# Kernel optimization log

Measured on AMD Instinct MI355X. Metric: run time of the kernel, lower is better.

The kernel has to match this reference:

```python
import jax, jax.numpy as jnp
import numpy as np

N = 50000   # nodes
E = 600000  # edges (avg degree 12)
D = 128     # embedding dim (hardcoded in original: np.zeros(128))
P = 5       # propagation iterations (self.p)


def setup_inputs() -> dict:
    key = jax.random.key(0)
    ks = jax.random.split(key, 10)
    x = jax.random.normal(ks[0], (N, D), jnp.float32)
    g = jax.random.normal(ks[1], (D,), jnp.float32)
    dist = jax.random.uniform(ks[2], (E,), jnp.float32)
    w1 = jax.random.normal(ks[3], (1,), jnp.float32)
    w2 = jax.random.normal(ks[4], (1,), jnp.float32)
    w3 = jax.random.normal(ks[5], (1,), jnp.float32)
    w4 = jax.random.normal(ks[6], (1,), jnp.float32)
    w5 = jax.random.normal(ks[7], (1,), jnp.float32)
    src = jax.random.randint(ks[8], (E,), 0, N)
    dst = jax.random.randint(ks[9], (E,), 0, N)
    return {"x": x, "g": g, "dist": dist, "w1": w1, "w2": w2, "w3": w3,
            "w4": w4, "w5": w5, "src": src, "dst": dst}


def reference(x, g, dist, w1, w2, w3, w4, w5, src, dst):
    # travel_times[i] = sum_{j in N(i)} w5 * dist(i,j)  -- iteration-invariant
    travel = jax.ops.segment_sum(w5[0] * dist, src, num_segments=N)  # [N]
    # per-node affine part, constant across the P iterations
    base = w1[0] * x + w2[0] * g[None, :] + w4[0] * jax.nn.relu(travel)[:, None]  # [N, D]
    u = x  # new_u_vect starts as a copy of x
    for _ in range(P):
        # u_sum[i] = sum_{j in N(i)} u[j]  (gather + segment-sum, synchronous update)
        u_sum = jax.ops.segment_sum(u[dst], src, num_segments=N)  # [N, D]
        u = base + w3[0] * u_sum
    return jax.nn.relu(u)
```

## Files before the change

### kernel.cpp

```cpp
#include <hip/hip_runtime.h>

#define D 128
#define D4 32
#define CAPH 32

typedef float v4f __attribute__((ext_vector_type(4)));
typedef _Float16 h4 __attribute__((ext_vector_type(4)));

static inline size_t align_up(size_t v, size_t a) { return (v + a - 1) & ~(a - 1); }

__global__ void fill_ell_kernel(const int* __restrict__ src,
                                const int* __restrict__ dst,
                                const float* __restrict__ dist,
                                unsigned long long* __restrict__ packedA,
                                unsigned long long* __restrict__ packedB,
                                unsigned short* __restrict__ adjA,
                                unsigned short* __restrict__ adjB,
                                int E, int Ehalf) {
  int e = blockIdx.x * blockDim.x + threadIdx.x;
  if (e >= E) return;
  int s = src[e];
  unsigned long long fx = (unsigned long long)(dist[e] * 4294967296.0f);
  unsigned long long val = (1ull << 48) | fx;
  if (e < Ehalf) {
    unsigned long long old = atomicAdd(&packedA[s], val);
    unsigned int slot = (unsigned int)(old >> 48);
    if (slot < CAPH) adjA[(size_t)s * CAPH + slot] = (unsigned short)dst[e];
  } else {
    unsigned long long old = atomicAdd(&packedB[s], val);
    unsigned int slot = (unsigned int)(old >> 48);
    if (slot < CAPH) adjB[(size_t)s * CAPH + slot] = (unsigned short)dst[e];
  }
}

__global__ void base_seed_kernel(const v4f* __restrict__ x4, const v4f* __restrict__ g4,
                                 const unsigned long long* __restrict__ packedA,
                                 const unsigned long long* __restrict__ packedB,
                                 const float* __restrict__ w1p, const float* __restrict__ w2p,
                                 const float* __restrict__ w4p, const float* __restrict__ w5p,
                                 h4* __restrict__ base, h4* __restrict__ uA,
                                 h4* __restrict__ uB, int n) {
  int i = blockIdx.x * blockDim.x + threadIdx.x;
  int node = i >> 5;
  int lane = i & 31;
  if (node > n) return;
  size_t idx = (size_t)i;
  if (node == n) {
    h4 z = {0, 0, 0, 0};
    uA[idx] = z;
    uB[idx] = z;
    return;
  }
  v4f xv = x4[(size_t)node * D4 + lane];
  v4f gv = g4[lane];
  unsigned long long sum = (packedA[node] & 0xFFFFFFFFFFFFull)
                         + (packedB[node] & 0xFFFFFFFFFFFFull);
  float ds = (float)sum * (1.0f / 4294967296.0f);
  float t = w5p[0] * ds;
  t = t > 0.f ? t : 0.f;
  v4f b = w1p[0] * xv + w2p[0] * gv;
  b += t * w4p[0];
  base[idx] = __builtin_convertvector(b, h4);
  uA[idx] = __builtin_convertvector(xv, h4);
}

__global__ __launch_bounds__(256) void prop_kernel(
    const h4* __restrict__ uin, const h4* __restrict__ base,
    const unsigned long long* __restrict__ packedA,
    const unsigned long long* __restrict__ packedB,
    const unsigned short* __restrict__ adjA,
    const unsigned short* __restrict__ adjB,
    const float* __restrict__ w3p,
    void* __restrict__ uout, int n, int final_relu)
{
  int half  = blockIdx.x & 1;
  int chunk = blockIdx.x >> 1;
  int group = threadIdx.x >> 4;
  int lane  = threadIdx.x & 15;
  int node  = chunk * 16 + group;
  if (node >= n) return;

  unsigned long long pA = packedA[node];
  unsigned long long pB = packedB[node];
  int degA = (int)(pA >> 48); if (degA > CAPH) degA = CAPH;
  int degB = (int)(pB >> 48); if (degB > CAPH) degB = CAPH;

  const unsigned short* rowA = adjA + (size_t)node * CAPH;
  const unsigned short* rowB = adjB + (size_t)node * CAPH;
  int a0 = rowA[lane];
  int a1 = rowA[lane + 16];
  int b0 = rowB[lane];
  int b1 = rowB[lane + 16];

  const h4* uh = uin + (size_t)half * 16 + lane;
  size_t idx = (size_t)node * 32 + half * 16 + lane;
  v4f bb = __builtin_convertvector(base[idx], v4f);

  v4f acc0 = {0.f,0.f,0.f,0.f}, acc1 = acc0, acc2 = acc0, acc3 = acc0;

  {
    int jA0 = __shfl(a0, 0, 16); jA0 = (0 < degA) ? jA0 : n;
    int jA1 = __shfl(a0, 1, 16); jA1 = (1 < degA) ? jA1 : n;
    int jA2 = __shfl(a0, 2, 16); jA2 = (2 < degA) ? jA2 : n;
    int jA3 = __shfl(a0, 3, 16); jA3 = (3 < degA) ? jA3 : n;
    int jA4 = __shfl(a0, 4, 16); jA4 = (4 < degA) ? jA4 : n;
    int jA5 = __shfl(a0, 5, 16); jA5 = (5 < degA) ? jA5 : n;
    int jA6 = __shfl(a0, 6, 16); jA6 = (6 < degA) ? jA6 : n;
    int jA7 = __shfl(a0, 7, 16); jA7 = (7 < degA) ? jA7 : n;
    int jB0 = __shfl(b0, 0, 16); jB0 = (0 < degB) ? jB0 : n;
    int jB1 = __shfl(b0, 1, 16); jB1 = (1 < degB) ? jB1 : n;
    int jB2 = __shfl(b0, 2, 16); jB2 = (2 < degB) ? jB2 : n;
    int jB3 = __shfl(b0, 3, 16); jB3 = (3 < degB) ? jB3 : n;
    int jB4 = __shfl(b0, 4, 16); jB4 = (4 < degB) ? jB4 : n;
    int jB5 = __shfl(b0, 5, 16); jB5 = (5 < degB) ? jB5 : n;
    int jB6 = __shfl(b0, 6, 16); jB6 = (6 < degB) ? jB6 : n;
    int jB7 = __shfl(b0, 7, 16); jB7 = (7 < degB) ? jB7 : n;
    h4 vA0 = uh[(size_t)jA0 * 32];
    h4 vA1 = uh[(size_t)jA1 * 32];
    h4 vA2 = uh[(size_t)jA2 * 32];
    h4 vA3 = uh[(size_t)jA3 * 32];
    h4 vA4 = uh[(size_t)jA4 * 32];
    h4 vA5 = uh[(size_t)jA5 * 32];
    h4 vA6 = uh[(size_t)jA6 * 32];
    h4 vA7 = uh[(size_t)jA7 * 32];
    h4 vB0 = uh[(size_t)jB0 * 32];
    h4 vB1 = uh[(size_t)jB1 * 32];
    h4 vB2 = uh[(size_t)jB2 * 32];
    h4 vB3 = uh[(size_t)jB3 * 32];
    h4 vB4 = uh[(size_t)jB4 * 32];
    h4 vB5 = uh[(size_t)jB5 * 32];
    h4 vB6 = uh[(size_t)jB6 * 32];
    h4 vB7 = uh[(size_t)jB7 * 32];
    acc0 += __builtin_convertvector(vA0, v4f) + __builtin_convertvector(vA1, v4f);
    acc1 += __builtin_convertvector(vA2, v4f) + __builtin_convertvector(vA3, v4f);
    acc2 += __builtin_convertvector(vA4, v4f) + __builtin_convertvector(vA5, v4f);
    acc3 += __builtin_convertvector(vA6, v4f) + __builtin_convertvector(vA7, v4f);
    acc0 += __builtin_convertvector(vB0, v4f) + __builtin_convertvector(vB1, v4f);
    acc1 += __builtin_convertvector(vB2, v4f) + __builtin_convertvector(vB3, v4f);
    acc2 += __builtin_convertvector(vB4, v4f) + __builtin_convertvector(vB5, v4f);
    acc3 += __builtin_convertvector(vB6, v4f) + __builtin_convertvector(vB7, v4f);
  }

  for (int k = 8; k < degA; k += 8) {
    int sel = (k >= 16) ? a1 : a0;
    int j0 = __shfl(sel, (k + 0) & 15, 16); j0 = (k + 0 < degA) ? j0 : n;
    int j1 = __shfl(sel, (k + 1) & 15, 16); j1 = (k + 1 < degA) ? j1 : n;
    int j2 = __shfl(sel, (k + 2) & 15, 16); j2 = (k + 2 < degA) ? j2 : n;
    int j3 = __shfl(sel, (k + 3) & 15, 16); j3 = (k + 3 < degA) ? j3 : n;
    int j4 = __shfl(sel, (k + 4) & 15, 16); j4 = (k + 4 < degA) ? j4 : n;
    int j5 = __shfl(sel, (k + 5) & 15, 16); j5 = (k + 5 < degA) ? j5 : n;
    int j6 = __shfl(sel, (k + 6) & 15, 16); j6 = (k + 6 < degA) ? j6 : n;
    int j7 = __shfl(sel, (k + 7) & 15, 16); j7 = (k + 7 < degA) ? j7 : n;
    h4 v0 = uh[(size_t)j0 * 32];
    h4 v1 = uh[(size_t)j1 * 32];
    h4 v2 = uh[(size_t)j2 * 32];
    h4 v3 = uh[(size_t)j3 * 32];
    h4 v4 = uh[(size_t)j4 * 32];
    h4 v5 = uh[(size_t)j5 * 32];
    h4 v6 = uh[(size_t)j6 * 32];
    h4 v7 = uh[(size_t)j7 * 32];
    acc0 += __builtin_convertvector(v0, v4f) + __builtin_convertvector(v1, v4f);
    acc1 += __builtin_convertvector(v2, v4f) + __builtin_convertvector(v3, v4f);
    acc2 += __builtin_convertvector(v4, v4f) + __builtin_convertvector(v5, v4f);
    acc3 += __builtin_convertvector(v6, v4f) + __builtin_convertvector(v7, v4f);
  }
  for (int k = 8; k < degB; k += 8) {
    int sel = (k >= 16) ? b1 : b0;
    int j0 = __shfl(sel, (k + 0) & 15, 16); j0 = (k + 0 < degB) ? j0 : n;
    int j1 = __shfl(sel, (k + 1) & 15, 16); j1 = (k + 1 < degB) ? j1 : n;
    int j2 = __shfl(sel, (k + 2) & 15, 16); j2 = (k + 2 < degB) ? j2 : n;
    int j3 = __shfl(sel, (k + 3) & 15, 16); j3 = (k + 3 < degB) ? j3 : n;
    int j4 = __shfl(sel, (k + 4) & 15, 16); j4 = (k + 4 < degB) ? j4 : n;
    int j5 = __shfl(sel, (k + 5) & 15, 16); j5 = (k + 5 < degB) ? j5 : n;
    int j6 = __shfl(sel, (k + 6) & 15, 16); j6 = (k + 6 < degB) ? j6 : n;
    int j7 = __shfl(sel, (k + 7) & 15, 16); j7 = (k + 7 < degB) ? j7 : n;
    h4 v0 = uh[(size_t)j0 * 32];
    h4 v1 = uh[(size_t)j1 * 32];
    h4 v2 = uh[(size_t)j2 * 32];
    h4 v3 = uh[(size_t)j3 * 32];
    h4 v4 = uh[(size_t)j4 * 32];
    h4 v5 = uh[(size_t)j5 * 32];
    h4 v6 = uh[(size_t)j6 * 32];
    h4 v7 = uh[(size_t)j7 * 32];
    acc0 += __builtin_convertvector(v0, v4f) + __builtin_convertvector(v1, v4f);
    acc1 += __builtin_convertvector(v2, v4f) + __builtin_convertvector(v3, v4f);
    acc2 += __builtin_convertvector(v4, v4f) + __builtin_convertvector(v5, v4f);
    acc3 += __builtin_convertvector(v6, v4f) + __builtin_convertvector(v7, v4f);
  }
  v4f asum = (acc0 + acc1) + (acc2 + acc3);
  v4f r = bb + w3p[0] * asum;

  if (final_relu) {
    r.x = r.x > 0.f ? r.x : 0.f;
    r.y = r.y > 0.f ? r.y : 0.f;
    r.z = r.z > 0.f ? r.z : 0.f;
    r.w = r.w > 0.f ? r.w : 0.f;
    __builtin_nontemporal_store(r, (v4f*)uout + idx);
  } else {
    ((h4*)uout)[idx] = __builtin_convertvector(r, h4);
  }
}

extern "C" void kernel_launch(void* const* d_in, const int* in_sizes, int n_in,
                              void* d_out, int out_size, void* d_ws, size_t ws_size,
                              hipStream_t stream) {
  const float* x    = (const float*)d_in[0];
  const float* g    = (const float*)d_in[1];
  const float* dist = (const float*)d_in[2];
  const float* w1   = (const float*)d_in[3];
  const float* w2   = (const float*)d_in[4];
  const float* w3   = (const float*)d_in[5];
  const float* w4   = (const float*)d_in[6];
  const float* w5   = (const float*)d_in[7];
  const int*   src  = (const int*)d_in[8];
  const int*   dst  = (const int*)d_in[9];

  const int N = in_sizes[0] / D;
  const int E = in_sizes[2];
  const int Ehalf = E / 2;

  char* ws = (char*)d_ws;
  size_t o = 0;
  unsigned long long* packedA = (unsigned long long*)(ws + o); o += align_up((size_t)N * 8, 256);
  unsigned long long* packedB = (unsigned long long*)(ws + o);
  size_t zero_end = o + (size_t)N * 8;
  o += align_up((size_t)N * 8, 256);
  unsigned short* adjA = (unsigned short*)(ws + o); o += align_up((size_t)N * CAPH * 2, 256);
  unsigned short* adjB = (unsigned short*)(ws + o); o += align_up((size_t)N * CAPH * 2, 256);
  h4* baseB = (h4*)(ws + o); o += align_up((size_t)(N + 1) * D * 2, 256);
  h4* uA    = (h4*)(ws + o); o += align_up((size_t)(N + 1) * D * 2, 256);
  h4* uB    = (h4*)(ws + o); o += align_up((size_t)(N + 1) * D * 2, 256);
  float* out = (float*)d_out;

  hipMemsetAsync(ws, 0, zero_end, stream);

  const int tb = 256;
  const int eblocks = (E + tb - 1) / tb;
  const int sthreads = (N + 1) * 32;
  const int sblocks = (sthreads + tb - 1) / tb;

  fill_ell_kernel<<<eblocks, tb, 0, stream>>>(src, dst, dist, packedA, packedB,
                                              adjA, adjB, E, Ehalf);
  base_seed_kernel<<<sblocks, tb, 0, stream>>>((const v4f*)x, (const v4f*)g,
                                               packedA, packedB,
                                               w1, w2, w4, w5, baseB, uA, uB, N);

  const int chunks = (N + 15) / 16;
  const int pblocks = chunks * 2;
  prop_kernel<<<pblocks, 256, 0, stream>>>(uA, baseB, packedA, packedB, adjA, adjB, w3, uB,  N, 0);
  prop_kernel<<<pblocks, 256, 0, stream>>>(uB, baseB, packedA, packedB, adjA, adjB, w3, uA,  N, 0);
  prop_kernel<<<pblocks, 256, 0, stream>>>(uA, baseB, packedA, packedB, adjA, adjB, w3, uB,  N, 0);
  prop_kernel<<<pblocks, 256, 0, stream>>>(uB, baseB, packedA, packedB, adjA, adjB, w3, uA,  N, 0);
  prop_kernel<<<pblocks, 256, 0, stream>>>(uA, baseB, packedA, packedB, adjA, adjB, w3, out, N, 1);
}
```

Before: 252.6 us.

## Fuse five propagation launches into one persistent kernel with grid barrier

Replaces the five per-iteration prop_kernel launches with one persistent kernel of 768 blocks. Each block owns several node chunks and keeps their adjacency indices, degrees and base values in registers across all iterations. Iterations are separated by an atomic-counter grid barrier held in a zeroed workspace region. This removes launch gaps and repeated loads of per-node metadata, but relies on all 768 blocks being co-resident, which the launch-bounds hint of 3 blocks per CU is meant to ensure. It also raises register pressure and reduces parallelism per iteration.

```diff
diff --git a/kernel.cpp b/kernel.cpp
--- a/kernel.cpp
+++ b/kernel.cpp
@@ -3,6 +3,9 @@
 #define D 128
 #define D4 32
 #define CAPH 32
+#define PITER 5
+#define GBLK 768
+#define CHUNKS 9
 
 typedef float v4f __attribute__((ext_vector_type(4)));
 typedef _Float16 h4 __attribute__((ext_vector_type(4)));
@@ -64,140 +67,180 @@
   uA[idx] = __builtin_convertvector(xv, h4);
 }
 
-__global__ __launch_bounds__(256) void prop_kernel(
-    const h4* __restrict__ uin, const h4* __restrict__ base,
+__global__ __launch_bounds__(256, 3) void prop_persist_kernel(
+    h4* __restrict__ uAb, h4* __restrict__ uBb,
+    const h4* __restrict__ base,
     const unsigned long long* __restrict__ packedA,
     const unsigned long long* __restrict__ packedB,
     const unsigned short* __restrict__ adjA,
     const unsigned short* __restrict__ adjB,
     const float* __restrict__ w3p,
-    void* __restrict__ uout, int n, int final_relu)
+    unsigned* __restrict__ bar,
+    float* __restrict__ out, int n)
 {
   int half  = blockIdx.x & 1;
-  int chunk = blockIdx.x >> 1;
+  int bp    = blockIdx.x >> 1;
   int group = threadIdx.x >> 4;
   int lane  = threadIdx.x & 15;
-  int node  = chunk * 16 + group;
-  if (node >= n) return;
-
-  unsigned long long pA = packedA[node];
-  unsigned long long pB = packedB[node];
-  int degA = (int)(pA >> 48); if (degA > CAPH) degA = CAPH;
-  int degB = (int)(pB >> 48); if (degB > CAPH) degB = CAPH;
-
-  const unsigned short* rowA = adjA + (size_t)node * CAPH;
-  const unsigned short* rowB = adjB + (size_t)node * CAPH;
-  int a0 = rowA[lane];
-  int a1 = rowA[lane + 16];
-  int b0 = rowB[lane];
-  int b1 = rowB[lane + 16];
-
-  const h4* uh = uin + (size_t)half * 16 + lane;
-  size_t idx = (size_t)node * 32 + half * 16 + lane;
-  v4f bb = __builtin_convertvector(base[idx], v4f);
-
-  v4f acc0 = {0.f,0.f,0.f,0.f}, acc1 = acc0, acc2 = acc0, acc3 = acc0;
-
-  {
-    int jA0 = __shfl(a0, 0, 16); jA0 = (0 < degA) ? jA0 : n;
-    int jA1 = __shfl(a0, 1, 16); jA1 = (1 < degA) ? jA1 : n;
-    int jA2 = __shfl(a0, 2, 16); jA2 = (2 < degA) ? jA2 : n;
-    int jA3 = __shfl(a0, 3, 16); jA3 = (3 < degA) ? jA3 : n;
-    int jA4 = __shfl(a0, 4, 16); jA4 = (4 < degA) ? jA4 : n;
-    int jA5 = __shfl(a0, 5, 16); jA5 = (5 < degA) ? jA5 : n;
-    int jA6 = __shfl(a0, 6, 16); jA6 = (6 < degA) ? jA6 : n;
-    int jA7 = __shfl(a0, 7, 16); jA7 = (7 < degA) ? jA7 : n;
-    int jB0 = __shfl(b0, 0, 16); jB0 = (0 < degB) ? jB0 : n;
-    int jB1 = __shfl(b0, 1, 16); jB1 = (1 < degB) ? jB1 : n;
-    int jB2 = __shfl(b0, 2, 16); jB2 = (2 < degB) ? jB2 : n;
-    int jB3 = __shfl(b0, 3, 16); jB3 = (3 < degB) ? jB3 : n;
-    int jB4 = __shfl(b0, 4, 16); jB4 = (4 < degB) ? jB4 : n;
-    int jB5 = __shfl(b0, 5, 16); jB5 = (5 < degB) ? jB5 : n;
-    int jB6 = __shfl(b0, 6, 16); jB6 = (6 < degB) ? jB6 : n;
-    int jB7 = __shfl(b0, 7, 16); jB7 = (7 < degB) ? jB7 : n;
-    h4 vA0 = uh[(size_t)jA0 * 32];
-    h4 vA1 = uh[(size_t)jA1 * 32];
-    h4 vA2 = uh[(size_t)jA2 * 32];
-    h4 vA3 = uh[(size_t)jA3 * 32];
-    h4 vA4 = uh[(size_t)jA4 * 32];
-    h4 vA5 = uh[(size_t)jA5 * 32];
-    h4 vA6 = uh[(size_t)jA6 * 32];
-    h4 vA7 = uh[(size_t)jA7 * 32];
-    h4 vB0 = uh[(size_t)jB0 * 32];
-    h4 vB1 = uh[(size_t)jB1 * 32];
-    h4 vB2 = uh[(size_t)jB2 * 32];
-    h4 vB3 = uh[(size_t)jB3 * 32];
-    h4 vB4 = uh[(size_t)jB4 * 32];
-    h4 vB5 = uh[(size_t)jB5 * 32];
-    h4 vB6 = uh[(size_t)jB6 * 32];
-    h4 vB7 = uh[(size_t)jB7 * 32];
-    acc0 += __builtin_convertvector(vA0, v4f) + __builtin_convertvector(vA1, v4f);
-    acc1 += __builtin_convertvector(vA2, v4f) + __builtin_convertvector(vA3, v4f);
-    acc2 += __builtin_convertvector(vA4, v4f) + __builtin_convertvector(vA5, v4f);
-    acc3 += __builtin_convertvector(vA6, v4f) + __builtin_convertvector(vA7, v4f);
-    acc0 += __builtin_convertvector(vB0, v4f) + __builtin_convertvector(vB1, v4f);
-    acc1 += __builtin_convertvector(vB2, v4f) + __builtin_convertvector(vB3, v4f);
-    acc2 += __builtin_convertvector(vB4, v4f) + __builtin_convertvector(vB5, v4f);
-    acc3 += __builtin_convertvector(vB6, v4f) + __builtin_convertvector(vB7, v4f);
-  }
-
-  for (int k = 8; k < degA; k += 8) {
-    int sel = (k >= 16) ? a1 : a0;
-    int j0 = __shfl(sel, (k + 0) & 15, 16); j0 = (k + 0 < degA) ? j0 : n;
-    int j1 = __shfl(sel, (k + 1) & 15, 16); j1 = (k + 1 < degA) ? j1 : n;
-    int j2 = __shfl(sel, (k + 2) & 15, 16); j2 = (k + 2 < degA) ? j2 : n;
-    int j3 = __shfl(sel, (k + 3) & 15, 16); j3 = (k + 3 < degA) ? j3 : n;
-    int j4 = __shfl(sel, (k + 4) & 15, 16); j4 = (k + 4 < degA) ? j4 : n;
-    int j5 = __shfl(sel, (k + 5) & 15, 16); j5 = (k + 5 < degA) ? j5 : n;
-    int j6 = __shfl(sel, (k + 6) & 15, 16); j6 = (k + 6 < degA) ? j6 : n;
-    int j7 = __shfl(sel, (k + 7) & 15, 16); j7 = (k + 7 < degA) ? j7 : n;
-    h4 v0 = uh[(size_t)j0 * 32];
-    h4 v1 = uh[(size_t)j1 * 32];
-    h4 v2 = uh[(size_t)j2 * 32];
-    h4 v3 = uh[(size_t)j3 * 32];
-    h4 v4 = uh[(size_t)j4 * 32];
-    h4 v5 = uh[(size_t)j5 * 32];
-    h4 v6 = uh[(size_t)j6 * 32];
-    h4 v7 = uh[(size_t)j7 * 32];
-    acc0 += __builtin_convertvector(v0, v4f) + __builtin_convertvector(v1, v4f);
-    acc1 += __builtin_convertvector(v2, v4f) + __builtin_convertvector(v3, v4f);
-    acc2 += __builtin_convertvector(v4, v4f) + __builtin_convertvector(v5, v4f);
-    acc3 += __builtin_convertvector(v6, v4f) + __builtin_convertvector(v7, v4f);
-  }
-  for (int k = 8; k < degB; k += 8) {
-    int sel = (k >= 16) ? b1 : b0;
-    int j0 = __shfl(sel, (k + 0) & 15, 16); j0 = (k + 0 < degB) ? j0 : n;
-    int j1 = __shfl(sel, (k + 1) & 15, 16); j1 = (k + 1 < degB) ? j1 : n;
-    int j2 = __shfl(sel, (k + 2) & 15, 16); j2 = (k + 2 < degB) ? j2 : n;
-    int j3 = __shfl(sel, (k + 3) & 15, 16); j3 = (k + 3 < degB) ? j3 : n;
-    int j4 = __shfl(sel, (k + 4) & 15, 16); j4 = (k + 4 < degB) ? j4 : n;
-    int j5 = __shfl(sel, (k + 5) & 15, 16); j5 = (k + 5 < degB) ? j5 : n;
-    int j6 = __shfl(sel, (k + 6) & 15, 16); j6 = (k + 6 < degB) ? j6 : n;
-    int j7 = __shfl(sel, (k + 7) & 15, 16); j7 = (k + 7 < degB) ? j7 : n;
-    h4 v0 = uh[(size_t)j0 * 32];
-    h4 v1 = uh[(size_t)j1 * 32];
-    h4 v2 = uh[(size_t)j2 * 32];
-    h4 v3 = uh[(size_t)j3 * 32];
-    h4 v4 = uh[(size_t)j4 * 32];
-    h4 v5 = uh[(size_t)j5 * 32];
-    h4 v6 = uh[(size_t)j6 * 32];
-    h4 v7 = uh[(size_t)j7 * 32];
-    acc0 += __builtin_convertvector(v0, v4f) + __builtin_convertvector(v1, v4f);
-    acc1 += __builtin_convertvector(v2, v4f) + __builtin_convertvector(v3, v4f);
-    acc2 += __builtin_convertvector(v4, v4f) + __builtin_convertvector(v5, v4f);
-    acc3 += __builtin_convertvector(v6, v4f) + __builtin_convertvector(v7, v4f);
-  }
-  v4f asum = (acc0 + acc1) + (acc2 + acc3);
-  v4f r = bb + w3p[0] * asum;
-
-  if (final_relu) {
-    r.x = r.x > 0.f ? r.x : 0.f;
-    r.y = r.y > 0.f ? r.y : 0.f;
-    r.z = r.z > 0.f ? r.z : 0.f;
-    r.w = r.w > 0.f ? r.w : 0.f;
-    __builtin_nontemporal_store(r, (v4f*)uout + idx);
-  } else {
-    ((h4*)uout)[idx] = __builtin_convertvector(r, h4);
+  int gg    = bp * 16 + group;
+  const int stride = (GBLK >> 1) * 16;
+
+  float w3 = w3p[0];
+
+  int a0[CHUNKS], a1[CHUNKS], b0[CHUNKS], b1[CHUNKS];
+  int dgA[CHUNKS], dgB[CHUNKS];
+  h4 bs[CHUNKS];
+#pragma unroll
+  for (int c = 0; c < CHUNKS; ++c) {
+    int node = gg + c * stride;
+    bool valid = node < n;
+    int nd = valid ? node : 0;
+    unsigned long long pA = packedA[nd];
+    unsigned long long pB = packedB[nd];
+    int dA = (int)(pA >> 48); if (dA > CAPH) dA = CAPH;
+    int dB = (int)(pB >> 48); if (dB > CAPH) dB = CAPH;
+    dgA[c] = valid ? dA : 0;
+    dgB[c] = valid ? dB : 0;
+    const unsigned short* rowA = adjA + (size_t)nd * CAPH;
+    const unsigned short* rowB = adjB + (size_t)nd * CAPH;
+    a0[c] = rowA[lane];
+    a1[c] = rowA[lane + 16];
+    b0[c] = rowB[lane];
+    b1[c] = rowB[lane + 16];
+    bs[c] = base[(size_t)nd * 32 + half * 16 + lane];
+  }
+
+  for (int it = 0; it < PITER; ++it) {
+    const h4* uin = (it & 1) ? uBb : uAb;
+    h4* uoutp     = (it & 1) ? uAb : uBb;
+    const h4* uh  = uin + (size_t)half * 16 + lane;
+    int last = (it == PITER - 1);
+
+#pragma unroll
+    for (int c = 0; c < CHUNKS; ++c) {
+      int node = gg + c * stride;
+      if (node >= n) break;
+      int degA = dgA[c];
+      int degB = dgB[c];
+
+      v4f acc0 = {0.f,0.f,0.f,0.f}, acc1 = acc0, acc2 = acc0, acc3 = acc0;
+
+      {
+        int jA0 = __shfl(a0[c], 0, 16); jA0 = (0 < degA) ? jA0 : n;
+        int jA1 = __shfl(a0[c], 1, 16); jA1 = (1 < degA) ? jA1 : n;
+        int jA2 = __shfl(a0[c], 2, 16); jA2 = (2 < degA) ? jA2 : n;
+        int jA3 = __shfl(a0[c], 3, 16); jA3 = (3 < degA) ? jA3 : n;
+        int jA4 = __shfl(a0[c], 4, 16); jA4 = (4 < degA) ? jA4 : n;
+        int jA5 = __shfl(a0[c], 5, 16); jA5 = (5 < degA) ? jA5 : n;
+        int jA6 = __shfl(a0[c], 6, 16); jA6 = (6 < degA) ? jA6 : n;
+        int jA7 = __shfl(a0[c], 7, 16); jA7 = (7 < degA) ? jA7 : n;
+        int jB0 = __shfl(b0[c], 0, 16); jB0 = (0 < degB) ? jB0 : n;
+        int jB1 = __shfl(b0[c], 1, 16); jB1 = (1 < degB) ? jB1 : n;
+        int jB2 = __shfl(b0[c], 2, 16); jB2 = (2 < degB) ? jB2 : n;
+        int jB3 = __shfl(b0[c], 3, 16); jB3 = (3 < degB) ? jB3 : n;
+        int jB4 = __shfl(b0[c], 4, 16); jB4 = (4 < degB) ? jB4 : n;
+        int jB5 = __shfl(b0[c], 5, 16); jB5 = (5 < degB) ? jB5 : n;
+        int jB6 = __shfl(b0[c], 6, 16); jB6 = (6 < degB) ? jB6 : n;
+        int jB7 = __shfl(b0[c], 7, 16); jB7 = (7 < degB) ? jB7 : n;
+        h4 vA0 = uh[(size_t)jA0 * 32];
+        h4 vA1 = uh[(size_t)jA1 * 32];
+        h4 vA2 = uh[(size_t)jA2 * 32];
+        h4 vA3 = uh[(size_t)jA3 * 32];
+        h4 vA4 = uh[(size_t)jA4 * 32];
+        h4 vA5 = uh[(size_t)jA5 * 32];
+        h4 vA6 = uh[(size_t)jA6 * 32];
+        h4 vA7 = uh[(size_t)jA7 * 32];
+        h4 vB0 = uh[(size_t)jB0 * 32];
+        h4 vB1 = uh[(size_t)jB1 * 32];
+        h4 vB2 = uh[(size_t)jB2 * 32];
+        h4 vB3 = uh[(size_t)jB3 * 32];
+        h4 vB4 = uh[(size_t)jB4 * 32];
+        h4 vB5 = uh[(size_t)jB5 * 32];
+        h4 vB6 = uh[(size_t)jB6 * 32];
+        h4 vB7 = uh[(size_t)jB7 * 32];
+        acc0 += __builtin_convertvector(vA0, v4f) + __builtin_convertvector(vA1, v4f);
+        acc1 += __builtin_convertvector(vA2, v4f) + __builtin_convertvector(vA3, v4f);
+        acc2 += __builtin_convertvector(vA4, v4f) + __builtin_convertvector(vA5, v4f);
+        acc3 += __builtin_convertvector(vA6, v4f) + __builtin_convertvector(vA7, v4f);
+        acc0 += __builtin_convertvector(vB0, v4f) + __builtin_convertvector(vB1, v4f);
+        acc1 += __builtin_convertvector(vB2, v4f) + __builtin_convertvector(vB3, v4f);
+        acc2 += __builtin_convertvector(vB4, v4f) + __builtin_convertvector(vB5, v4f);
+        acc3 += __builtin_convertvector(vB6, v4f) + __builtin_convertvector(vB7, v4f);
+      }
+
+      for (int k = 8; k < degA; k += 8) {
+        int sel = (k >= 16) ? a1[c] : a0[c];
+        int j0 = __shfl(sel, (k + 0) & 15, 16); j0 = (k + 0 < degA) ? j0 : n;
+        int j1 = __shfl(sel, (k + 1) & 15, 16); j1 = (k + 1 < degA) ? j1 : n;
+        int j2 = __shfl(sel, (k + 2) & 15, 16); j2 = (k + 2 < degA) ? j2 : n;
+        int j3 = __shfl(sel, (k + 3) & 15, 16); j3 = (k + 3 < degA) ? j3 : n;
+        int j4 = __shfl(sel, (k + 4) & 15, 16); j4 = (k + 4 < degA) ? j4 : n;
+        int j5 = __shfl(sel, (k + 5) & 15, 16); j5 = (k + 5 < degA) ? j5 : n;
+        int j6 = __shfl(sel, (k + 6) & 15, 16); j6 = (k + 6 < degA) ? j6 : n;
+        int j7 = __shfl(sel, (k + 7) & 15, 16); j7 = (k + 7 < degA) ? j7 : n;
+        h4 v0 = uh[(size_t)j0 * 32];
+        h4 v1 = uh[(size_t)j1 * 32];
+        h4 v2 = uh[(size_t)j2 * 32];
+        h4 v3 = uh[(size_t)j3 * 32];
+        h4 v4 = uh[(size_t)j4 * 32];
+        h4 v5 = uh[(size_t)j5 * 32];
+        h4 v6 = uh[(size_t)j6 * 32];
+        h4 v7 = uh[(size_t)j7 * 32];
+        acc0 += __builtin_convertvector(v0, v4f) + __builtin_convertvector(v1, v4f);
+        acc1 += __builtin_convertvector(v2, v4f) + __builtin_convertvector(v3, v4f);
+        acc2 += __builtin_convertvector(v4, v4f) + __builtin_convertvector(v5, v4f);
+        acc3 += __builtin_convertvector(v6, v4f) + __builtin_convertvector(v7, v4f);
+      }
+      for (int k = 8; k < degB; k += 8) {
+        int sel = (k >= 16) ? b1[c] : b0[c];
+        int j0 = __shfl(sel, (k + 0) & 15, 16); j0 = (k + 0 < degB) ? j0 : n;
+        int j1 = __shfl(sel, (k + 1) & 15, 16); j1 = (k + 1 < degB) ? j1 : n;
+        int j2 = __shfl(sel, (k + 2) & 15, 16); j2 = (k + 2 < degB) ? j2 : n;
+        int j3 = __shfl(sel, (k + 3) & 15, 16); j3 = (k + 3 < degB) ? j3 : n;
+        int j4 = __shfl(sel, (k + 4) & 15, 16); j4 = (k + 4 < degB) ? j4 : n;
+        int j5 = __shfl(sel, (k + 5) & 15, 16); j5 = (k + 5 < degB) ? j5 : n;
+        int j6 = __shfl(sel, (k + 6) & 15, 16); j6 = (k + 6 < degB) ? j6 : n;
+        int j7 = __shfl(sel, (k + 7) & 15, 16); j7 = (k + 7 < degB) ? j7 : n;
+        h4 v0 = uh[(size_t)j0 * 32];
+        h4 v1 = uh[(size_t)j1 * 32];
+        h4 v2 = uh[(size_t)j2 * 32];
+        h4 v3 = uh[(size_t)j3 * 32];
+        h4 v4 = uh[(size_t)j4 * 32];
+        h4 v5 = uh[(size_t)j5 * 32];
+        h4 v6 = uh[(size_t)j6 * 32];
+        h4 v7 = uh[(size_t)j7 * 32];
+        acc0 += __builtin_convertvector(v0, v4f) + __builtin_convertvector(v1, v4f);
+        acc1 += __builtin_convertvector(v2, v4f) + __builtin_convertvector(v3, v4f);
+        acc2 += __builtin_convertvector(v4, v4f) + __builtin_convertvector(v5, v4f);
+        acc3 += __builtin_convertvector(v6, v4f) + __builtin_convertvector(v7, v4f);
+      }
+
+      v4f asum = (acc0 + acc1) + (acc2 + acc3);
+      v4f r = __builtin_convertvector(bs[c], v4f) + w3 * asum;
+      size_t idx = (size_t)node * 32 + half * 16 + lane;
+      if (last) {
+        r.x = r.x > 0.f ? r.x : 0.f;
+        r.y = r.y > 0.f ? r.y : 0.f;
+        r.z = r.z > 0.f ? r.z : 0.f;
+        r.w = r.w > 0.f ? r.w : 0.f;
+        __builtin_nontemporal_store(r, (v4f*)out + idx);
+      } else {
+        uoutp[idx] = __builtin_convertvector(r, h4);
+      }
+    }
+
+    if (!last) {
+      __syncthreads();
+      if (threadIdx.x == 0) {
+        __threadfence();
+        atomicAdd(&bar[it], 1u);
+        while (__hip_atomic_load(&bar[it], __ATOMIC_RELAXED,
+                                 __HIP_MEMORY_SCOPE_AGENT) < (unsigned)GBLK)
+          __builtin_amdgcn_s_sleep(2);
+        __threadfence();
+      }
+      __syncthreads();
+    }
   }
 }
 
@@ -222,9 +265,10 @@
   char* ws = (char*)d_ws;
   size_t o = 0;
   unsigned long long* packedA = (unsigned long long*)(ws + o); o += align_up((size_t)N * 8, 256);
-  unsigned long long* packedB = (unsigned long long*)(ws + o);
-  size_t zero_end = o + (size_t)N * 8;
-  o += align_up((size_t)N * 8, 256);
+  unsigned long long* packedB = (unsigned long long*)(ws + o); o += align_up((size_t)N * 8, 256);
+  unsigned* bar = (unsigned*)(ws + o);
+  size_t zero_end = o + 256;
+  o += 256;
   unsigned short* adjA = (unsigned short*)(ws + o); o += align_up((size_t)N * CAPH * 2, 256);
   unsigned short* adjB = (unsigned short*)(ws + o); o += align_up((size_t)N * CAPH * 2, 256);
   h4* baseB = (h4*)(ws + o); o += align_up((size_t)(N + 1) * D * 2, 256);
@@ -245,11 +289,6 @@
                                                packedA, packedB,
                                                w1, w2, w4, w5, baseB, uA, uB, N);
 
-  const int chunks = (N + 15) / 16;
-  const int pblocks = chunks * 2;
-  prop_kernel<<<pblocks, 256, 0, stream>>>(uA, baseB, packedA, packedB, adjA, adjB, w3, uB,  N, 0);
-  prop_kernel<<<pblocks, 256, 0, stream>>>(uB, baseB, packedA, packedB, adjA, adjB, w3, uA,  N, 0);
-  prop_kernel<<<pblocks, 256, 0, stream>>>(uA, baseB, packedA, packedB, adjA, adjB, w3, uB,  N, 0);
-  prop_kernel<<<pblocks, 256, 0, stream>>>(uB, baseB, packedA, packedB, adjA, adjB, w3, uA,  N, 0);
-  prop_kernel<<<pblocks, 256, 0, stream>>>(uA, baseB, packedA, packedB, adjA, adjB, w3, out, N, 1);
-}
+  prop_persist_kernel<<<GBLK, 256, 0, stream>>>(uA, uB, baseB, packedA, packedB,
+                                                adjA, adjB, w3, bar, out, N);
+}
```

Result: slower. 667.7 us (+164.3%).
